# Kernel optimization log

Hardware: AMD Instinct MI355X
Metric: run time of the kernel (lower is better)

Reference implementation:

```python
import jax, jax.numpy as jnp
import numpy as np

T, H, I, E, K = 4096, 2048, 4096, 8, 2

def setup_inputs() -> dict:
    key = jax.random.key(0)
    k1, k2, k3, k4, k5 = jax.random.split(key, 5)
    return {
        "hidden_states": jax.random.normal(k1, (T, H), dtype=jnp.float32),
        "topk_weights": jax.random.uniform(k2, (T, K), dtype=jnp.float32, minval=0.01, maxval=1.0),
        "topk_ids": jax.random.randint(k3, (T, K), 0, E, dtype=jnp.int64),
        "gate_up_weights": jax.random.normal(k4, (E, 2 * I, H), dtype=jnp.float32) * 0.02,
        "down_weights": jax.random.normal(k5, (E, H, I), dtype=jnp.float32) * 0.02,
    }

def reference(hidden_states, topk_weights, topk_ids, gate_up_weights, down_weights):
    # renormalize=True: per-token top-k weights sum to 1
    tw = topk_weights / jnp.sum(topk_weights, axis=-1, keepdims=True)  # [T, K]
    n_experts = gate_up_weights.shape[0]
    # per-expert combine weight for each token: sum of tw where routed to expert e -> [E, T]
    expert_w = jax.vmap(
        lambda e: jnp.sum(jnp.where(topk_ids == e, tw, 0.0), axis=-1)
    )(jnp.arange(n_experts))

    def body(acc, ew):
        gu, dw, w = ew  # gu: [2I, H], dw: [H, I], w: [T]
        h = hidden_states @ gu.T            # [T, 2I]
        gate, up = jnp.split(h, 2, axis=-1)  # silu_and_mul epilogue
        act = jax.nn.silu(gate) * up        # [T, I]
        out_e = act @ dw.T                  # [T, H]
        return acc + w[:, None] * out_e, None

    init = jnp.zeros_like(hidden_states)
    out, _ = jax.lax.scan(body, init, (gate_up_weights, down_weights, expert_w))
    return out
```

## Files before the change

### kernel.cpp

```cpp
#include <hip/hip_runtime.h>


#define T_TOK 4096
#define H_DIM 2048
#define I_DIM 4096
#define E_NUM 8
#define K_TOP 2
#define NSLOT (T_TOK * K_TOP)

#define BM 128
#define BN 128
#define BK 64
#define LDKO 72

typedef float f32x4 __attribute__((ext_vector_type(4)));
typedef __bf16 bf16x8 __attribute__((ext_vector_type(8)));
typedef unsigned int u32x4 __attribute__((ext_vector_type(4)));

static __device__ __forceinline__ unsigned short f2bf(float f) {
  unsigned u = __float_as_uint(f);
  u += 0x7FFFu + ((u >> 16) & 1u);
  return (unsigned short)(u >> 16);
}

static __device__ __forceinline__ unsigned long long pack4bf(float x0, float x1, float x2, float x3) {
  unsigned lo = (unsigned)f2bf(x0) | ((unsigned)f2bf(x1) << 16);
  unsigned hi = (unsigned)f2bf(x2) | ((unsigned)f2bf(x3) << 16);
  return (unsigned long long)lo | ((unsigned long long)hi << 32);
}

static __device__ __forceinline__ void gload16(void* lds, const void* g) {
  __builtin_amdgcn_global_load_lds(
      (const __attribute__((address_space(1))) unsigned int*)(g),
      (__attribute__((address_space(3))) unsigned int*)(lds), 16, 0, 0);
}

__global__ void routing_kernel(const float* __restrict__ tw,
                               const int* __restrict__ ids,
                               int* __restrict__ offsets,
                               int* __restrict__ stok,
                               float* __restrict__ sw,
                               int* __restrict__ slot_of) {
  __shared__ int cnt[E_NUM];
  __shared__ int cur[E_NUM];
  __shared__ int basesh[E_NUM + 1];
  int tid = threadIdx.x;
  if (tid < E_NUM) cnt[tid] = 0;
  __syncthreads();
  for (int idx = tid; idx < NSLOT; idx += 256) atomicAdd(&cnt[ids[idx]], 1);
  __syncthreads();
  if (tid == 0) {
    int acc = 0;
    for (int e = 0; e < E_NUM; ++e) { basesh[e] = acc; acc += cnt[e]; }
    basesh[E_NUM] = acc;
    for (int e = 0; e <= E_NUM; ++e) offsets[e] = basesh[e];
  }
  __syncthreads();
  if (tid < E_NUM) cur[tid] = basesh[tid];
  __syncthreads();
  for (int idx = tid; idx < NSLOT; idx += 256) {
    int t = idx >> 1;
    float w0 = tw[t * 2], w1 = tw[t * 2 + 1];
    float w = ((idx & 1) ? w1 : w0) / (w0 + w1);
    int e = ids[idx];
    int slot = atomicAdd(&cur[e], 1);
    stok[slot] = t;
    sw[slot] = w;
    slot_of[idx] = slot;
  }
}

__global__ __launch_bounds__(256) void cvt_bf16_kernel(const float* __restrict__ in,
                                                       unsigned short* __restrict__ out,
                                                       long long n8) {
  long long stride = (long long)gridDim.x * 256;
  for (long long i = (long long)blockIdx.x * 256 + threadIdx.x; i < n8; i += stride) {
    long long o = i * 8;
    f32x4 v0 = *(const f32x4*)(in + o);
    f32x4 v1 = *(const f32x4*)(in + o + 4);
    unsigned long long p0 = pack4bf(v0[0], v0[1], v0[2], v0[3]);
    unsigned long long p1 = pack4bf(v1[0], v1[1], v1[2], v1[3]);
    u32x4 st;
    st[0] = (unsigned)p0; st[1] = (unsigned)(p0 >> 32);
    st[2] = (unsigned)p1; st[3] = (unsigned)(p1 >> 32);
    *(u32x4*)(out + o) = st;
  }
}

__global__ __launch_bounds__(256, 2) void gemm1_bf16_kernel(
    const unsigned short* __restrict__ hb,
    const unsigned short* __restrict__ gub,
    const int* __restrict__ offsets, const int* __restrict__ stok,
    unsigned short* __restrict__ act) {
  int e = blockIdx.z;
  int base = offsets[e];
  int cnt = offsets[e + 1] - base;
  int m0 = blockIdx.y * BM;
  if (m0 >= cnt) return;
  int n0 = blockIdx.x * BN;
  int rem = cnt - m0;

  __shared__ __attribute__((aligned(16))) unsigned short As[BM * 64];
  __shared__ __attribute__((aligned(16))) unsigned short Bg[BN * 64];
  __shared__ __attribute__((aligned(16))) unsigned short Bu[BN * 64];
  __shared__ int toks[BM];

  int tid = threadIdx.x;
  if (tid < BM) toks[tid] = (tid < rem) ? stok[base + m0 + tid] : stok[base];
  __syncthreads();

  int lane = tid & 63;
  int wid = tid >> 6;
  int srow = lane >> 3;
  int scol = ((lane & 7) ^ srow) << 3;

  const unsigned short* wrow = gub + (size_t)e * (2 * (size_t)I_DIM) * H_DIM;
  const unsigned short* pa[4];
  const unsigned short* pg[4];
  const unsigned short* pu[4];
#pragma unroll
  for (int s = 0; s < 4; ++s) {
    int row = wid * 32 + s * 8 + srow;
    pa[s] = hb + (size_t)toks[row] * H_DIM + scol;
    pg[s] = wrow + (size_t)(n0 + row) * H_DIM + scol;
    pu[s] = wrow + (size_t)(I_DIM + n0 + row) * H_DIM + scol;
  }

  int lm = lane & 15;
  int q = lane >> 4;
  int wm = (wid >> 1) * 64;
  int wn = (wid & 1) * 64;
  int rc0 = ((q ^ (lm & 7)) << 3);
  int rc1 = (((4 + q) ^ (lm & 7)) << 3);

  f32x4 accg[4][4] = {};
  f32x4 accu[4][4] = {};

  for (int kb = 0; kb < H_DIM; kb += BK) {
#pragma unroll
    for (int s = 0; s < 4; ++s) {
      gload16(&As[(wid * 32 + s * 8) * 64], pa[s] + kb);
      gload16(&Bg[(wid * 32 + s * 8) * 64], pg[s] + kb);
      gload16(&Bu[(wid * 32 + s * 8) * 64], pu[s] + kb);
    }
    __syncthreads();
#pragma unroll
    for (int ks = 0; ks < 2; ++ks) {
      int ko = ks ? rc1 : rc0;
      bf16x8 a[4], bg[4], bu[4];
#pragma unroll
      for (int i = 0; i < 4; ++i)
        a[i] = *(const bf16x8*)&As[(wm + i * 16 + lm) * 64 + ko];
#pragma unroll
      for (int j = 0; j < 4; ++j) {
        bg[j] = *(const bf16x8*)&Bg[(wn + j * 16 + lm) * 64 + ko];
        bu[j] = *(const bf16x8*)&Bu[(wn + j * 16 + lm) * 64 + ko];
      }
#pragma unroll
      for (int i = 0; i < 4; ++i)
#pragma unroll
        for (int j = 0; j < 4; ++j) {
          accg[i][j] = __builtin_amdgcn_mfma_f32_16x16x32_bf16(a[i], bg[j], accg[i][j], 0, 0, 0);
          accu[i][j] = __builtin_amdgcn_mfma_f32_16x16x32_bf16(a[i], bu[j], accu[i][j], 0, 0, 0);
        }
    }
    __syncthreads();
  }

#pragma unroll
  for (int i = 0; i < 4; ++i) {
    int mb = wm + i * 16 + q * 4;
#pragma unroll
    for (int r = 0; r < 4; ++r) {
      int m = mb + r;
      if (m < rem) {
        size_t rowoff = (size_t)(base + m0 + m) * I_DIM + n0;
#pragma unroll
        for (int j = 0; j < 4; ++j) {
          int n = wn + j * 16 + lm;
          float g = accg[i][j][r];
          float u = accu[i][j][r];
          float aa = (g / (1.0f + __expf(-g))) * u;
          act[rowoff + n] = f2bf(aa);
        }
      }
    }
  }
}

__global__ __launch_bounds__(256, 3) void gemm2_bf16_kernel(
    const unsigned short* __restrict__ act, const unsigned short* __restrict__ dwb,
    const int* __restrict__ offsets, const float* __restrict__ sw,
    float* __restrict__ dout) {
  int e = blockIdx.z;
  int base = offsets[e];
  int cnt = offsets[e + 1] - base;
  int m0 = blockIdx.y * BM;
  if (m0 >= cnt) return;
  int n0 = blockIdx.x * BN;
  int rem = cnt - m0;

  __shared__ __attribute__((aligned(16))) unsigned short As[BM * 64];
  __shared__ __attribute__((aligned(16))) unsigned short Bs[BN * 64];
  __shared__ float wsl[BM];

  int tid = threadIdx.x;
  if (tid < BM) wsl[tid] = (tid < rem) ? sw[base + m0 + tid] : 0.f;

  int lane = tid & 63;
  int wid = tid >> 6;
  int srow = lane >> 3;
  int scol = ((lane & 7) ^ srow) << 3;

  const unsigned short* dp = dwb + (size_t)e * ((size_t)H_DIM * I_DIM);
  const unsigned short* pa[4];
  const unsigned short* pb[4];
#pragma unroll
  for (int s = 0; s < 4; ++s) {
    int row = wid * 32 + s * 8 + srow;
    pa[s] = act + (size_t)(base + m0 + row) * I_DIM + scol;
    pb[s] = dp + (size_t)(n0 + row) * I_DIM + scol;
  }

  int lm = lane & 15;
  int q = lane >> 4;
  int wm = (wid >> 1) * 64;
  int wn = (wid & 1) * 64;
  int rc0 = ((q ^ (lm & 7)) << 3);
  int rc1 = (((4 + q) ^ (lm & 7)) << 3);

  f32x4 acc[4][4] = {};

  for (int kb = 0; kb < I_DIM; kb += BK) {
#pragma unroll
    for (int s = 0; s < 4; ++s) {
      gload16(&As[(wid * 32 + s * 8) * 64], pa[s] + kb);
      gload16(&Bs[(wid * 32 + s * 8) * 64], pb[s] + kb);
    }
    __syncthreads();
#pragma unroll
    for (int ks = 0; ks < 2; ++ks) {
      int ko = ks ? rc1 : rc0;
      bf16x8 a[4], b[4];
#pragma unroll
      for (int i = 0; i < 4; ++i)
        a[i] = *(const bf16x8*)&As[(wm + i * 16 + lm) * 64 + ko];
#pragma unroll
      for (int j = 0; j < 4; ++j)
        b[j] = *(const bf16x8*)&Bs[(wn + j * 16 + lm) * 64 + ko];
#pragma unroll
      for (int i = 0; i < 4; ++i)
#pragma unroll
        for (int j = 0; j < 4; ++j)
          acc[i][j] = __builtin_amdgcn_mfma_f32_16x16x32_bf16(a[i], b[j], acc[i][j], 0, 0, 0);
    }
    __syncthreads();
  }

#pragma unroll
  for (int i = 0; i < 4; ++i) {
    int mb = wm + i * 16 + q * 4;
#pragma unroll
    for (int r = 0; r < 4; ++r) {
      int m = mb + r;
      if (m < rem) {
        float w = wsl[m];
        size_t rowoff = (size_t)(base + m0 + m) * H_DIM + n0;
#pragma unroll
        for (int j = 0; j < 4; ++j)
          dout[rowoff + wn + j * 16 + lm] = acc[i][j][r] * w;
      }
    }
  }
}

__global__ __launch_bounds__(256, 2) void gemm1_kernel(
    const float* __restrict__ hidden, const float* __restrict__ gu,
    const int* __restrict__ offsets, const int* __restrict__ stok,
    unsigned short* __restrict__ act) {
  int e = blockIdx.z;
  int base = offsets[e];
  int cnt = offsets[e + 1] - base;
  int m0 = blockIdx.y * BM;
  if (m0 >= cnt) return;
  int n0 = blockIdx.x * BN;
  int rem = cnt - m0;

  __shared__ unsigned short As[BM * LDKO];
  __shared__ unsigned short Bg[BM * LDKO];
  __shared__ unsigned short Bu[BM * LDKO];
  __shared__ int toks[BM];

  int tid = threadIdx.x;
  if (tid < BM) toks[tid] = (tid < rem) ? stok[base + m0 + tid] : -1;
  __syncthreads();

  int lane = tid & 63;
  int wid = tid >> 6;
  int wm = (wid >> 1) * 64;
  int wn = (wid & 1) * 64;
  int lm = lane & 15;
  int q = lane >> 4;

  f32x4 accg[4][4] = {};
  f32x4 accu[4][4] = {};
  const float* gup = gu + (size_t)e * (2 * (size_t)I_DIM * H_DIM);

  for (int kb = 0; kb < H_DIM; kb += 64) {
#pragma unroll
    for (int s = 0; s < 8; ++s) {
      int task = tid + s * 256;
      int row = task >> 4;
      int cg = (task & 15) << 2;
      int tok = toks[row];
      float x0 = 0.f, x1 = 0.f, x2 = 0.f, x3 = 0.f;
      if (tok >= 0) {
        f32x4 v = *(const f32x4*)(hidden + (size_t)tok * H_DIM + kb + cg);
        x0 = v[0]; x1 = v[1]; x2 = v[2]; x3 = v[3];
      }
      *(unsigned long long*)&As[row * LDKO + cg] = pack4bf(x0, x1, x2, x3);
    }
#pragma unroll
    for (int s = 0; s < 8; ++s) {
      int task = tid + s * 256;
      int row = task >> 4;
      int cg = (task & 15) << 2;
      f32x4 vg = *(const f32x4*)(gup + (size_t)(n0 + row) * H_DIM + kb + cg);
      f32x4 vu = *(const f32x4*)(gup + (size_t)(I_DIM + n0 + row) * H_DIM + kb + cg);
      *(unsigned long long*)&Bg[row * LDKO + cg] = pack4bf(vg[0], vg[1], vg[2], vg[3]);
      *(unsigned long long*)&Bu[row * LDKO + cg] = pack4bf(vu[0], vu[1], vu[2], vu[3]);
    }
    __syncthreads();
#pragma unroll
    for (int ks = 0; ks < 2; ++ks) {
      int ko = ks * 32 + q * 8;
      bf16x8 a[4], bg[4], bu[4];
#pragma unroll
      for (int i = 0; i < 4; ++i)
        a[i] = *(const bf16x8*)&As[(wm + i * 16 + lm) * LDKO + ko];
#pragma unroll
      for (int j = 0; j < 4; ++j) {
        bg[j] = *(const bf16x8*)&Bg[(wn + j * 16 + lm) * LDKO + ko];
        bu[j] = *(const bf16x8*)&Bu[(wn + j * 16 + lm) * LDKO + ko];
      }
#pragma unroll
      for (int i = 0; i < 4; ++i)
#pragma unroll
        for (int j = 0; j < 4; ++j) {
          accg[i][j] = __builtin_amdgcn_mfma_f32_16x16x32_bf16(a[i], bg[j], accg[i][j], 0, 0, 0);
          accu[i][j] = __builtin_amdgcn_mfma_f32_16x16x32_bf16(a[i], bu[j], accu[i][j], 0, 0, 0);
        }
    }
    __syncthreads();
  }

#pragma unroll
  for (int i = 0; i < 4; ++i) {
    int mb = wm + i * 16 + q * 4;
#pragma unroll
    for (int r = 0; r < 4; ++r) {
      int m = mb + r;
      if (m < rem) {
        size_t rowoff = (size_t)(base + m0 + m) * I_DIM + n0;
#pragma unroll
        for (int j = 0; j < 4; ++j) {
          int n = wn + j * 16 + lm;
          float g = accg[i][j][r];
          float u = accu[i][j][r];
          float aa = (g / (1.0f + __expf(-g))) * u;
          act[rowoff + n] = f2bf(aa);
        }
      }
    }
  }
}

__global__ __launch_bounds__(256, 2) void gemm2_kernel(
    const unsigned short* __restrict__ act, const float* __restrict__ dwn,
    const int* __restrict__ offsets, const float* __restrict__ sw,
    float* __restrict__ dout) {
  int e = blockIdx.z;
  int base = offsets[e];
  int cnt = offsets[e + 1] - base;
  int m0 = blockIdx.y * BM;
  if (m0 >= cnt) return;
  int n0 = blockIdx.x * BN;
  int rem = cnt - m0;

  __shared__ unsigned short As[BM * LDKO];
  __shared__ unsigned short Bs[BM * LDKO];
  __shared__ float wsl[BM];

  int tid = threadIdx.x;
  if (tid < BM) wsl[tid] = (tid < rem) ? sw[base + m0 + tid] : 0.f;

  int lane = tid & 63;
  int wid = tid >> 6;
  int wm = (wid >> 1) * 64;
  int wn = (wid & 1) * 64;
  int lm = lane & 15;
  int q = lane >> 4;

  f32x4 acc[4][4] = {};
  const float* dp = dwn + (size_t)e * ((size_t)H_DIM * I_DIM);
  const unsigned short* ap = act + (size_t)(base + m0) * I_DIM;

  for (int kb = 0; kb < I_DIM; kb += 64) {
#pragma unroll
    for (int s = 0; s < 4; ++s) {
      int task = tid + s * 256;
      int row = task >> 3;
      int cg = (task & 7) << 3;
      u32x4 v = *(const u32x4*)(ap + (size_t)row * I_DIM + kb + cg);
      *(u32x4*)&As[row * LDKO + cg] = v;
    }
#pragma unroll
    for (int s = 0; s < 8; ++s) {
      int task = tid + s * 256;
      int row = task >> 4;
      int cg = (task & 15) << 2;
      f32x4 v = *(const f32x4*)(dp + (size_t)(n0 + row) * I_DIM + kb + cg);
      *(unsigned long long*)&Bs[row * LDKO + cg] = pack4bf(v[0], v[1], v[2], v[3]);
    }
    __syncthreads();
#pragma unroll
    for (int ks = 0; ks < 2; ++ks) {
      int ko = ks * 32 + q * 8;
      bf16x8 a[4], b[4];
#pragma unroll
      for (int i = 0; i < 4; ++i)
        a[i] = *(const bf16x8*)&As[(wm + i * 16 + lm) * LDKO + ko];
#pragma unroll
      for (int j = 0; j < 4; ++j)
        b[j] = *(const bf16x8*)&Bs[(wn + j * 16 + lm) * LDKO + ko];
#pragma unroll
      for (int i = 0; i < 4; ++i)
#pragma unroll
        for (int j = 0; j < 4; ++j)
          acc[i][j] = __builtin_amdgcn_mfma_f32_16x16x32_bf16(a[i], b[j], acc[i][j], 0, 0, 0);
    }
    __syncthreads();
  }

#pragma unroll
  for (int i = 0; i < 4; ++i) {
    int mb = wm + i * 16 + q * 4;
#pragma unroll
    for (int r = 0; r < 4; ++r) {
      int m = mb + r;
      if (m < rem) {
        float w = wsl[m];
        size_t rowoff = (size_t)(base + m0 + m) * H_DIM + n0;
#pragma unroll
        for (int j = 0; j < 4; ++j)
          dout[rowoff + wn + j * 16 + lm] = acc[i][j][r] * w;
      }
    }
  }
}

__global__ void combine_kernel(const f32x4* __restrict__ dout4,
                               const int* __restrict__ slot_of,
                               f32x4* __restrict__ out4) {
  int idx = blockIdx.x * 256 + threadIdx.x;
  int t = idx >> 9;
  int c = idx & 511;
  int s0 = slot_of[t * 2];
  int s1 = slot_of[t * 2 + 1];
  f32x4 r = dout4[(size_t)s0 * 512 + c] + dout4[(size_t)s1 * 512 + c];
  out4[idx] = r;
}

extern "C" void kernel_launch(void* const* d_in, const int* in_sizes, int n_in,
                              void* d_out, int out_size, void* d_ws, size_t ws_size,
                              hipStream_t stream) {
  const float* hidden = (const float*)d_in[0];
  const float* tw     = (const float*)d_in[1];
  const int*   ids    = (const int*)d_in[2];
  const float* gu     = (const float*)d_in[3];
  const float* dwn    = (const float*)d_in[4];
  float* out = (float*)d_out;
  char* ws = (char*)d_ws;

  int*   offsets = (int*)ws;
  int*   stok    = (int*)(ws + 256);
  float* swp     = (float*)(ws + 256 + 32768);
  int*   slot_of = (int*)(ws + 256 + 65536);
  const size_t base_off = 1 << 17;
  const size_t act_sz   = (size_t)(NSLOT + BM) * I_DIM * 2;

  routing_kernel<<<1, 256, 0, stream>>>(tw, ids, offsets, stok, swp, slot_of);

  const size_t hb_sz  = (size_t)T_TOK * H_DIM * 2;
  const size_t gu_sz  = (size_t)E_NUM * 2 * (size_t)I_DIM * H_DIM * 2;
  const size_t dwn_sz = (size_t)E_NUM * (size_t)H_DIM * I_DIM * 2;
  const size_t w_off  = base_off + hb_sz;
  const size_t need   = w_off + gu_sz + act_sz;

  if (ws_size >= need) {
    unsigned short* hb   = (unsigned short*)(ws + base_off);
    unsigned short* gub  = (unsigned short*)(ws + w_off);
    unsigned short* dwb  = (unsigned short*)(ws + w_off);
    float*          dout = (float*)(ws + w_off + dwn_sz);
    unsigned short* act  = (unsigned short*)(ws + w_off + gu_sz);

    cvt_bf16_kernel<<<2048, 256, 0, stream>>>(hidden, hb, (long long)T_TOK * H_DIM / 8);
    cvt_bf16_kernel<<<2048, 256, 0, stream>>>(gu, gub, (long long)E_NUM * 2 * I_DIM * H_DIM / 8);
    gemm1_bf16_kernel<<<dim3(I_DIM / BN, NSLOT / BM, E_NUM), 256, 0, stream>>>(hb, gub, offsets, stok, act);
    cvt_bf16_kernel<<<2048, 256, 0, stream>>>(dwn, dwb, (long long)E_NUM * H_DIM * I_DIM / 8);
    gemm2_bf16_kernel<<<dim3(H_DIM / BN, NSLOT / BM, E_NUM), 256, 0, stream>>>(act, dwb, offsets, swp, dout);
    combine_kernel<<<(T_TOK * H_DIM / 4) / 256, 256, 0, stream>>>((const f32x4*)dout, slot_of, (f32x4*)out);
  } else {
    unsigned short* act  = (unsigned short*)(ws + base_off);
    float*          dout = (float*)(ws + base_off + act_sz);
    gemm1_kernel<<<dim3(I_DIM / BN, NSLOT / BM, E_NUM), 256, 0, stream>>>(hidden, gu, offsets, stok, act);
    gemm2_kernel<<<dim3(H_DIM / BN, NSLOT / BM, E_NUM), 256, 0, stream>>>(act, dwn, offsets, swp, dout);
    combine_kernel<<<(T_TOK * H_DIM / 4) / 256, 256, 0, stream>>>((const f32x4*)dout, slot_of, (f32x4*)out);
  }
}
```

Before: 1.481 ms.

## Double-buffer A tile in gate/up GEMM and widen K tile in down GEMM

In the gate/up GEMM, the gathered activation tile is now double-buffered. The next A tile is prefetched before the current compute, and explicit vmcnt waits and raw barriers replace __syncthreads, so gather latency overlaps with MFMA work. The down-projection GEMM doubles its K tile to 128 with a new swizzled load layout. This halves the loop iterations and barriers but doubles LDS use, which is why its occupancy hint drops from 3 to 2. The hand-written waitcnt counts are fragile, and the extra LDS may lower occupancy.

```diff
diff --git a/kernel.cpp b/kernel.cpp
--- a/kernel.cpp
+++ b/kernel.cpp
@@ -11,6 +11,7 @@
 #define BM 128
 #define BN 128
 #define BK 64
+#define BK2 128
 #define LDKO 72
 
 typedef float f32x4 __attribute__((ext_vector_type(4)));
@@ -100,7 +101,7 @@
   int n0 = blockIdx.x * BN;
   int rem = cnt - m0;
 
-  __shared__ __attribute__((aligned(16))) unsigned short As[BM * 64];
+  __shared__ __attribute__((aligned(16))) unsigned short As[2][BM * 64];
   __shared__ __attribute__((aligned(16))) unsigned short Bg[BN * 64];
   __shared__ __attribute__((aligned(16))) unsigned short Bu[BN * 64];
   __shared__ int toks[BM];
@@ -136,21 +137,36 @@
   f32x4 accg[4][4] = {};
   f32x4 accu[4][4] = {};
 
+#pragma unroll
+  for (int s = 0; s < 4; ++s)
+    gload16(&As[0][(wid * 32 + s * 8) * 64], pa[s]);
+
+  int cur = 0;
   for (int kb = 0; kb < H_DIM; kb += BK) {
 #pragma unroll
     for (int s = 0; s < 4; ++s) {
-      gload16(&As[(wid * 32 + s * 8) * 64], pa[s] + kb);
       gload16(&Bg[(wid * 32 + s * 8) * 64], pg[s] + kb);
       gload16(&Bu[(wid * 32 + s * 8) * 64], pu[s] + kb);
     }
-    __syncthreads();
+    if (kb + BK < H_DIM) {
+#pragma unroll
+      for (int s = 0; s < 4; ++s)
+        gload16(&As[cur ^ 1][(wid * 32 + s * 8) * 64], pa[s] + kb + BK);
+      __builtin_amdgcn_sched_barrier(0);
+      asm volatile("s_waitcnt vmcnt(4)" ::: "memory");
+    } else {
+      __builtin_amdgcn_sched_barrier(0);
+      asm volatile("s_waitcnt vmcnt(0)" ::: "memory");
+    }
+    __builtin_amdgcn_s_barrier();
+    __builtin_amdgcn_sched_barrier(0);
 #pragma unroll
     for (int ks = 0; ks < 2; ++ks) {
       int ko = ks ? rc1 : rc0;
       bf16x8 a[4], bg[4], bu[4];
 #pragma unroll
       for (int i = 0; i < 4; ++i)
-        a[i] = *(const bf16x8*)&As[(wm + i * 16 + lm) * 64 + ko];
+        a[i] = *(const bf16x8*)&As[cur][(wm + i * 16 + lm) * 64 + ko];
 #pragma unroll
       for (int j = 0; j < 4; ++j) {
         bg[j] = *(const bf16x8*)&Bg[(wn + j * 16 + lm) * 64 + ko];
@@ -164,7 +180,9 @@
           accu[i][j] = __builtin_amdgcn_mfma_f32_16x16x32_bf16(a[i], bu[j], accu[i][j], 0, 0, 0);
         }
     }
-    __syncthreads();
+    __builtin_amdgcn_sched_barrier(0);
+    __builtin_amdgcn_s_barrier();
+    cur ^= 1;
   }
 
 #pragma unroll
@@ -188,7 +206,7 @@
   }
 }
 
-__global__ __launch_bounds__(256, 3) void gemm2_bf16_kernel(
+__global__ __launch_bounds__(256, 2) void gemm2_bf16_kernel(
     const unsigned short* __restrict__ act, const unsigned short* __restrict__ dwb,
     const int* __restrict__ offsets, const float* __restrict__ sw,
     float* __restrict__ dout) {
@@ -200,8 +218,8 @@
   int n0 = blockIdx.x * BN;
   int rem = cnt - m0;
 
-  __shared__ __attribute__((aligned(16))) unsigned short As[BM * 64];
-  __shared__ __attribute__((aligned(16))) unsigned short Bs[BN * 64];
+  __shared__ __attribute__((aligned(16))) unsigned short As[BM * BK2];
+  __shared__ __attribute__((aligned(16))) unsigned short Bs[BM * BK2];
   __shared__ float wsl[BM];
 
   int tid = threadIdx.x;
@@ -209,45 +227,37 @@
 
   int lane = tid & 63;
   int wid = tid >> 6;
-  int srow = lane >> 3;
-  int scol = ((lane & 7) ^ srow) << 3;
+  int r0 = tid >> 4;
+  int cz = (((tid & 15) ^ r0) << 3);
 
   const unsigned short* dp = dwb + (size_t)e * ((size_t)H_DIM * I_DIM);
-  const unsigned short* pa[4];
-  const unsigned short* pb[4];
-#pragma unroll
-  for (int s = 0; s < 4; ++s) {
-    int row = wid * 32 + s * 8 + srow;
-    pa[s] = act + (size_t)(base + m0 + row) * I_DIM + scol;
-    pb[s] = dp + (size_t)(n0 + row) * I_DIM + scol;
-  }
+  const unsigned short* pa0 = act + (size_t)(base + m0 + r0) * I_DIM + cz;
+  const unsigned short* pb0 = dp + (size_t)(n0 + r0) * I_DIM + cz;
 
   int lm = lane & 15;
   int q = lane >> 4;
   int wm = (wid >> 1) * 64;
   int wn = (wid & 1) * 64;
-  int rc0 = ((q ^ (lm & 7)) << 3);
-  int rc1 = (((4 + q) ^ (lm & 7)) << 3);
 
   f32x4 acc[4][4] = {};
 
-  for (int kb = 0; kb < I_DIM; kb += BK) {
-#pragma unroll
-    for (int s = 0; s < 4; ++s) {
-      gload16(&As[(wid * 32 + s * 8) * 64], pa[s] + kb);
-      gload16(&Bs[(wid * 32 + s * 8) * 64], pb[s] + kb);
+  for (int kb = 0; kb < I_DIM; kb += BK2) {
+#pragma unroll
+    for (int s = 0; s < 8; ++s) {
+      gload16(&As[(s * 256 + tid) * 8], pa0 + (size_t)s * 16 * I_DIM + kb);
+      gload16(&Bs[(s * 256 + tid) * 8], pb0 + (size_t)s * 16 * I_DIM + kb);
     }
     __syncthreads();
 #pragma unroll
-    for (int ks = 0; ks < 2; ++ks) {
-      int ko = ks ? rc1 : rc0;
+    for (int ks = 0; ks < 4; ++ks) {
+      int ko = (((ks * 4 + q) ^ lm) << 3);
       bf16x8 a[4], b[4];
 #pragma unroll
       for (int i = 0; i < 4; ++i)
-        a[i] = *(const bf16x8*)&As[(wm + i * 16 + lm) * 64 + ko];
+        a[i] = *(const bf16x8*)&As[(wm + i * 16 + lm) * BK2 + ko];
 #pragma unroll
       for (int j = 0; j < 4; ++j)
-        b[j] = *(const bf16x8*)&Bs[(wn + j * 16 + lm) * 64 + ko];
+        b[j] = *(const bf16x8*)&Bs[(wn + j * 16 + lm) * BK2 + ko];
 #pragma unroll
       for (int i = 0; i < 4; ++i)
 #pragma unroll
```

After: 1.487 ms. Within noise of the previous version (+0.4%).

## Double-buffer the activation tile in both expert GEMMs to prefetch the next K-slice

Applied to the files above, without the earlier changes.

Both grouped GEMM kernels now keep two LDS buffers for the A operand (gathered token rows or activations). The next K-slice of A is issued before the current slice is consumed, and an explicit partial vmcnt wait retires only the current slice's loads. The intent is to hide the latency of the A loads, especially the token-indexed gather in the first GEMM, behind the MFMA work. The weight tile stays single-buffered and is still waited on within the same iteration. LDS use per block grows, and correctness now depends on hand-written waitcnt and barrier placement.

```diff
diff --git a/kernel.cpp b/kernel.cpp
--- a/kernel.cpp
+++ b/kernel.cpp
@@ -100,7 +100,7 @@
   int n0 = blockIdx.x * BN;
   int rem = cnt - m0;
 
-  __shared__ __attribute__((aligned(16))) unsigned short As[BM * 64];
+  __shared__ __attribute__((aligned(16))) unsigned short As[2][BM * 64];
   __shared__ __attribute__((aligned(16))) unsigned short Bg[BN * 64];
   __shared__ __attribute__((aligned(16))) unsigned short Bu[BN * 64];
   __shared__ int toks[BM];
@@ -136,21 +136,36 @@
   f32x4 accg[4][4] = {};
   f32x4 accu[4][4] = {};
 
+#pragma unroll
+  for (int s = 0; s < 4; ++s)
+    gload16(&As[0][(wid * 32 + s * 8) * 64], pa[s]);
+
+  int cur = 0;
   for (int kb = 0; kb < H_DIM; kb += BK) {
 #pragma unroll
     for (int s = 0; s < 4; ++s) {
-      gload16(&As[(wid * 32 + s * 8) * 64], pa[s] + kb);
       gload16(&Bg[(wid * 32 + s * 8) * 64], pg[s] + kb);
       gload16(&Bu[(wid * 32 + s * 8) * 64], pu[s] + kb);
     }
-    __syncthreads();
+    if (kb + BK < H_DIM) {
+#pragma unroll
+      for (int s = 0; s < 4; ++s)
+        gload16(&As[cur ^ 1][(wid * 32 + s * 8) * 64], pa[s] + kb + BK);
+      __builtin_amdgcn_sched_barrier(0);
+      asm volatile("s_waitcnt vmcnt(4)" ::: "memory");
+    } else {
+      __builtin_amdgcn_sched_barrier(0);
+      asm volatile("s_waitcnt vmcnt(0)" ::: "memory");
+    }
+    __builtin_amdgcn_s_barrier();
+    __builtin_amdgcn_sched_barrier(0);
 #pragma unroll
     for (int ks = 0; ks < 2; ++ks) {
       int ko = ks ? rc1 : rc0;
       bf16x8 a[4], bg[4], bu[4];
 #pragma unroll
       for (int i = 0; i < 4; ++i)
-        a[i] = *(const bf16x8*)&As[(wm + i * 16 + lm) * 64 + ko];
+        a[i] = *(const bf16x8*)&As[cur][(wm + i * 16 + lm) * 64 + ko];
 #pragma unroll
       for (int j = 0; j < 4; ++j) {
         bg[j] = *(const bf16x8*)&Bg[(wn + j * 16 + lm) * 64 + ko];
@@ -164,7 +179,9 @@
           accu[i][j] = __builtin_amdgcn_mfma_f32_16x16x32_bf16(a[i], bu[j], accu[i][j], 0, 0, 0);
         }
     }
-    __syncthreads();
+    __builtin_amdgcn_sched_barrier(0);
+    __builtin_amdgcn_s_barrier();
+    cur ^= 1;
   }
 
 #pragma unroll
@@ -200,12 +217,13 @@
   int n0 = blockIdx.x * BN;
   int rem = cnt - m0;
 
-  __shared__ __attribute__((aligned(16))) unsigned short As[BM * 64];
+  __shared__ __attribute__((aligned(16))) unsigned short As[2][BM * 64];
   __shared__ __attribute__((aligned(16))) unsigned short Bs[BN * 64];
   __shared__ float wsl[BM];
 
   int tid = threadIdx.x;
   if (tid < BM) wsl[tid] = (tid < rem) ? sw[base + m0 + tid] : 0.f;
+  __syncthreads();
 
   int lane = tid & 63;
   int wid = tid >> 6;
@@ -231,20 +249,34 @@
 
   f32x4 acc[4][4] = {};
 
+#pragma unroll
+  for (int s = 0; s < 4; ++s)
+    gload16(&As[0][(wid * 32 + s * 8) * 64], pa[s]);
+
+  int cur = 0;
   for (int kb = 0; kb < I_DIM; kb += BK) {
 #pragma unroll
-    for (int s = 0; s < 4; ++s) {
-      gload16(&As[(wid * 32 + s * 8) * 64], pa[s] + kb);
+    for (int s = 0; s < 4; ++s)
       gload16(&Bs[(wid * 32 + s * 8) * 64], pb[s] + kb);
-    }
-    __syncthreads();
+    if (kb + BK < I_DIM) {
+#pragma unroll
+      for (int s = 0; s < 4; ++s)
+        gload16(&As[cur ^ 1][(wid * 32 + s * 8) * 64], pa[s] + kb + BK);
+      __builtin_amdgcn_sched_barrier(0);
+      asm volatile("s_waitcnt vmcnt(4)" ::: "memory");
+    } else {
+      __builtin_amdgcn_sched_barrier(0);
+      asm volatile("s_waitcnt vmcnt(0)" ::: "memory");
+    }
+    __builtin_amdgcn_s_barrier();
+    __builtin_amdgcn_sched_barrier(0);
 #pragma unroll
     for (int ks = 0; ks < 2; ++ks) {
       int ko = ks ? rc1 : rc0;
       bf16x8 a[4], b[4];
 #pragma unroll
       for (int i = 0; i < 4; ++i)
-        a[i] = *(const bf16x8*)&As[(wm + i * 16 + lm) * 64 + ko];
+        a[i] = *(const bf16x8*)&As[cur][(wm + i * 16 + lm) * 64 + ko];
 #pragma unroll
       for (int j = 0; j < 4; ++j)
         b[j] = *(const bf16x8*)&Bs[(wn + j * 16 + lm) * 64 + ko];
@@ -254,7 +286,9 @@
         for (int j = 0; j < 4; ++j)
           acc[i][j] = __builtin_amdgcn_mfma_f32_16x16x32_bf16(a[i], b[j], acc[i][j], 0, 0, 0);
     }
-    __syncthreads();
+    __builtin_amdgcn_sched_barrier(0);
+    __builtin_amdgcn_s_barrier();
+    cur ^= 1;
   }
 
 #pragma unroll
```

Measured after the change: 1.452 ms (median of 3 runs). 1.02x faster.
